# Kernel tuning notes

Measured on AMD Instinct MI355X. Metric: run time of the kernel, lower is better.

Reference implementation:

```python
import jax, jax.numpy as jnp
import numpy as np

N_GAUSS, H, W, SH_DEG = 1024, 256, 256, 3

SH_C0 = 0.28209479177387814
SH_C1 = 0.4886025119029199
SH_C2 = (1.0925484305920792, -1.0925484305920792, 0.31539156525252005,
         -1.0925484305920792, 0.5462742152960396)
SH_C3 = (-0.5900435899266435, 2.890611442640554, -0.4570457994644658,
         0.3731763325901154, -0.4570457994644658, 1.445305721320277,
         -0.5900435899266435)


def eval_sh(shs, dirs):
    # shs: [N,16,3], dirs: [N,3] normalized. Matches computeColorFromSH (deg 3).
    x, y, z = dirs[:, 0:1], dirs[:, 1:2], dirs[:, 2:3]
    res = SH_C0 * shs[:, 0]
    res = res - SH_C1 * y * shs[:, 1] + SH_C1 * z * shs[:, 2] - SH_C1 * x * shs[:, 3]
    xx, yy, zz = x * x, y * y, z * z
    xy, yz, xz = x * y, y * z, x * z
    res = (res + SH_C2[0] * xy * shs[:, 4] + SH_C2[1] * yz * shs[:, 5]
           + SH_C2[2] * (2.0 * zz - xx - yy) * shs[:, 6]
           + SH_C2[3] * xz * shs[:, 7] + SH_C2[4] * (xx - yy) * shs[:, 8])
    res = (res + SH_C3[0] * y * (3.0 * xx - yy) * shs[:, 9]
           + SH_C3[1] * xy * z * shs[:, 10]
           + SH_C3[2] * y * (4.0 * zz - xx - yy) * shs[:, 11]
           + SH_C3[3] * z * (2.0 * zz - 3.0 * xx - 3.0 * yy) * shs[:, 12]
           + SH_C3[4] * x * (4.0 * zz - xx - yy) * shs[:, 13]
           + SH_C3[5] * z * (xx - yy) * shs[:, 14]
           + SH_C3[6] * x * (xx - yy - zz) * shs[:, 15])
    return jnp.maximum(res + 0.5, 0.0)


def render(background, means3D, opacities, scales, rotations, shs,
           view_mat, proj_mat, cam_pos, tan_fovx, tan_fovy, height, width):
    N = means3D.shape[0]
    tanx, tany = tan_fovx[0], tan_fovy[0]
    fx = width / (2.0 * tanx)
    fy = height / (2.0 * tany)

    # --- 3D covariance: Sigma = R diag(s^2) R^T (computeCov3D) ---
    q = rotations / jnp.linalg.norm(rotations, axis=-1, keepdims=True)
    r, x, y, z = q[:, 0], q[:, 1], q[:, 2], q[:, 3]
    R = jnp.stack([
        jnp.stack([1 - 2 * (y * y + z * z), 2 * (x * y - r * z), 2 * (x * z + r * y)], -1),
        jnp.stack([2 * (x * y + r * z), 1 - 2 * (x * x + z * z), 2 * (y * z - r * x)], -1),
        jnp.stack([2 * (x * z - r * y), 2 * (y * z + r * x), 1 - 2 * (x * x + y * y)], -1),
    ], -2)  # [N,3,3]
    M = R * scales[:, None, :]
    Sigma = jnp.einsum('nij,nkj->nik', M, M)  # [N,3,3]

    # --- view transform + EWA 2D covariance (computeCov2D) ---
    t = means3D @ view_mat[:3, :3].T + view_mat[:3, 3]  # [N,3] camera space
    tz = t[:, 2]
    valid_z = tz > 0.2
    tzs = jnp.where(valid_z, tz, 1.0)
    limx, limy = 1.3 * tanx, 1.3 * tany
    tx = jnp.clip(t[:, 0] / tzs, -limx, limx) * tzs
    ty = jnp.clip(t[:, 1] / tzs, -limy, limy) * tzs
    zeros = jnp.zeros_like(tzs)
    J = jnp.stack([
        jnp.stack([fx / tzs, zeros, -fx * tx / (tzs * tzs)], -1),
        jnp.stack([zeros, fy / tzs, -fy * ty / (tzs * tzs)], -1),
    ], -2)  # [N,2,3]
    T2 = jnp.einsum('nij,jk->nik', J, view_mat[:3, :3])
    cov2d = jnp.einsum('nij,njk,nlk->nil', T2, Sigma, T2)  # [N,2,2]
    a = cov2d[:, 0, 0] + 0.3
    c = cov2d[:, 1, 1] + 0.3
    b = cov2d[:, 0, 1]
    det = a * c - b * b
    valid = valid_z & (det > 0)
    inv_det = jnp.where(det > 0, 1.0 / jnp.where(det > 0, det, 1.0), 0.0)
    conic = jnp.stack([c, -b, a], -1) * inv_det[:, None]  # [N,3]

    # --- projection to pixel coords (ndc2Pix) ---
    ph = jnp.concatenate([means3D, jnp.ones((N, 1), means3D.dtype)], -1) @ proj_mat.T
    p_w = 1.0 / (ph[:, 3] + 1e-7)
    px = ((ph[:, 0] * p_w + 1.0) * width - 1.0) * 0.5
    py = ((ph[:, 1] * p_w + 1.0) * height - 1.0) * 0.5

    # --- SH -> RGB ---
    dirs = means3D - cam_pos[None, :]
    dirs = dirs / jnp.linalg.norm(dirs, axis=-1, keepdims=True)
    colors = eval_sh(shs, dirs)  # [N,3]

    # --- global depth sort (front to back) ---
    depth = jnp.where(valid, tz, 1e10)
    order = jnp.argsort(depth)
    px_s, py_s = px[order], py[order]
    conic_s = conic[order]
    opac_s = opacities[order, 0]
    colors_s = colors[order]
    valid_s = valid[order]

    # --- per-pixel alpha and front-to-back compositing (renderCUDA) ---
    ys, xs = jnp.meshgrid(jnp.arange(height, dtype=jnp.float32),
                          jnp.arange(width, dtype=jnp.float32), indexing='ij')
    pixx, pixy = xs.reshape(-1), ys.reshape(-1)  # [P]
    dx = px_s[:, None] - pixx[None, :]  # [N,P]
    dy = py_s[:, None] - pixy[None, :]
    power = (-0.5 * (conic_s[:, 0:1] * dx * dx + conic_s[:, 2:3] * dy * dy)
             - conic_s[:, 1:2] * dx * dy)
    alpha = jnp.minimum(opac_s[:, None] * jnp.exp(jnp.minimum(power, 0.0)), 0.99)
    keep = (power <= 0.0) & (alpha >= 1.0 / 255.0) & valid_s[:, None]
    alpha = jnp.where(keep, alpha, 0.0)

    Tcum = jnp.cumprod(1.0 - alpha, axis=0)  # [N,P]
    T_prev = jnp.concatenate([jnp.ones((1, alpha.shape[1]), alpha.dtype), Tcum[:-1]], 0)
    wgt = alpha * T_prev
    img = jnp.einsum('nc,np->cp', colors_s, wgt) + background[:, None] * Tcum[-1][None, :]
    return img.reshape(3, height, width)


def setup_inputs() -> dict:
    key = jax.random.key(0)
    ks = jax.random.split(key, 6)
    means3D = jax.random.uniform(ks[0], (N_GAUSS, 3), minval=-3.0, maxval=3.0)
    means3D = means3D.at[:, 2].set(
        jax.random.uniform(ks[1], (N_GAUSS,), minval=2.0, maxval=10.0))
    opacities = jax.random.uniform(ks[2], (N_GAUSS, 1), minval=0.3, maxval=0.95)
    scales = jax.random.uniform(ks[3], (N_GAUSS, 3), minval=0.02, maxval=0.15)
    rotations = jax.random.normal(ks[4], (N_GAUSS, 4))
    shs = jax.random.normal(ks[5], (N_GAUSS, (SH_DEG + 1) ** 2, 3)) * 0.3
    background = jnp.zeros((3,), jnp.float32)
    view_mat = jnp.eye(4, dtype=jnp.float32)  # camera at origin looking +z
    tanx = tany = 0.5
    zn, zf = 0.01, 100.0
    proj = np.zeros((4, 4), np.float32)
    proj[0, 0] = 1.0 / tanx
    proj[1, 1] = 1.0 / tany
    proj[2, 2] = zf / (zf - zn)
    proj[2, 3] = -(zf * zn) / (zf - zn)
    proj[3, 2] = 1.0
    proj_mat = jnp.asarray(proj) @ view_mat  # full projection
    cam_pos = jnp.zeros((3,), jnp.float32)
    return dict(background=background, means3D=means3D, opacities=opacities,
                scales=scales, rotations=rotations, shs=shs, view_mat=view_mat,
                proj_mat=proj_mat, cam_pos=cam_pos,
                tan_fovx=jnp.array([tanx], jnp.float32),
                tan_fovy=jnp.array([tany], jnp.float32), height=H, width=W)


def reference(background, means3D, opacities, scales, rotations, shs,
              view_mat, proj_mat, cam_pos, tan_fovx, tan_fovy, height, width):
    return render(background, means3D, opacities, scales, rotations, shs,
                  view_mat, proj_mat, cam_pos, tan_fovx, tan_fovy, height, width)
```

## Files before the change

kernel.cpp:

```cpp
#include <hip/hip_runtime.h>
#include <math.h>

#define NG 1024
#define LOG2E 1.4426950408889634f


__global__ void prep_kernel(
    const float* __restrict__ means3D, const float* __restrict__ opacities,
    const float* __restrict__ scales,  const float* __restrict__ rotations,
    const float* __restrict__ shs,     const float* __restrict__ view_mat,
    const float* __restrict__ proj_mat,const float* __restrict__ cam_pos,
    const float* __restrict__ tanx_p,  const float* __restrict__ tany_p,
    const int* __restrict__ h_p,       const int* __restrict__ w_p,
    unsigned long long* __restrict__ keys, float4* __restrict__ bbox,
    float4* __restrict__ rec, int N)
{
    int i = blockIdx.x * blockDim.x + threadIdx.x;
    if (i >= N) return;
    float tanx = tanx_p[0], tany = tany_p[0];
    float Wf = (float)w_p[0], Hf = (float)h_p[0];
    float fx = Wf / (2.f * tanx), fy = Hf / (2.f * tany);

    float mx = means3D[3*i], my = means3D[3*i+1], mz = means3D[3*i+2];

    float qr = rotations[4*i],   qx = rotations[4*i+1];
    float qy = rotations[4*i+2], qz = rotations[4*i+3];
    float qn = sqrtf(qr*qr + qx*qx + qy*qy + qz*qz);
    qr /= qn; qx /= qn; qy /= qn; qz /= qn;
    float sx = scales[3*i], sy = scales[3*i+1], sz = scales[3*i+2];
    float R00 = 1.f-2.f*(qy*qy+qz*qz), R01 = 2.f*(qx*qy-qr*qz), R02 = 2.f*(qx*qz+qr*qy);
    float R10 = 2.f*(qx*qy+qr*qz), R11 = 1.f-2.f*(qx*qx+qz*qz), R12 = 2.f*(qy*qz-qr*qx);
    float R20 = 2.f*(qx*qz-qr*qy), R21 = 2.f*(qy*qz+qr*qx), R22 = 1.f-2.f*(qx*qx+qy*qy);
    float M00=R00*sx, M01=R01*sy, M02=R02*sz;
    float M10=R10*sx, M11=R11*sy, M12=R12*sz;
    float M20=R20*sx, M21=R21*sy, M22=R22*sz;
    float S00 = M00*M00+M01*M01+M02*M02;
    float S01 = M00*M10+M01*M11+M02*M12;
    float S02 = M00*M20+M01*M21+M02*M22;
    float S11 = M10*M10+M11*M11+M12*M12;
    float S12 = M10*M20+M11*M21+M12*M22;
    float S22 = M20*M20+M21*M21+M22*M22;

    const float* V = view_mat;
    float t0 = V[0]*mx + V[1]*my + V[2]*mz  + V[3];
    float t1 = V[4]*mx + V[5]*my + V[6]*mz  + V[7];
    float t2 = V[8]*mx + V[9]*my + V[10]*mz + V[11];
    bool valid_z = t2 > 0.2f;
    float tzs = valid_z ? t2 : 1.0f;
    float limx = 1.3f*tanx, limy = 1.3f*tany;
    float txc = fminf(fmaxf(t0/tzs, -limx), limx) * tzs;
    float tyc = fminf(fmaxf(t1/tzs, -limy), limy) * tzs;
    float inv_tz = 1.f / tzs;
    float J00 = fx*inv_tz, J02 = -fx*txc*inv_tz*inv_tz;
    float J11 = fy*inv_tz, J12 = -fy*tyc*inv_tz*inv_tz;
    float T200 = J00*V[0] + J02*V[8];
    float T201 = J00*V[1] + J02*V[9];
    float T202 = J00*V[2] + J02*V[10];
    float T210 = J11*V[4] + J12*V[8];
    float T211 = J11*V[5] + J12*V[9];
    float T212 = J11*V[6] + J12*V[10];
    float u0 = S00*T200 + S01*T201 + S02*T202;
    float u1 = S01*T200 + S11*T201 + S12*T202;
    float u2 = S02*T200 + S12*T201 + S22*T202;
    float cov00 = T200*u0 + T201*u1 + T202*u2;
    float cov01 = T210*u0 + T211*u1 + T212*u2;
    float v0 = S00*T210 + S01*T211 + S02*T212;
    float v1 = S01*T210 + S11*T211 + S12*T212;
    float v2 = S02*T210 + S12*T211 + S22*T212;
    float cov11 = T210*v0 + T211*v1 + T212*v2;
    float a = cov00 + 0.3f;
    float c = cov11 + 0.3f;
    float b = cov01;
    float det = a*c - b*b;
    bool valid = valid_z && (det > 0.f);
    float inv_det = (det > 0.f) ? (1.f/det) : 0.f;
    float Aq = c*inv_det, Bq = -b*inv_det, Cq = a*inv_det;

    const float* P = proj_mat;
    float ph0 = P[0]*mx  + P[1]*my  + P[2]*mz  + P[3];
    float ph1 = P[4]*mx  + P[5]*my  + P[6]*mz  + P[7];
    float ph3 = P[12]*mx + P[13]*my + P[14]*mz + P[15];
    float pw = 1.f / (ph3 + 1e-7f);
    float px = ((ph0*pw + 1.f)*Wf - 1.f)*0.5f;
    float py = ((ph1*pw + 1.f)*Hf - 1.f)*0.5f;

    float dxm = mx - cam_pos[0], dym = my - cam_pos[1], dzm = mz - cam_pos[2];
    float dn = sqrtf(dxm*dxm + dym*dym + dzm*dzm);
    float X = dxm/dn, Y = dym/dn, Z = dzm/dn;
    float xx = X*X, yy = Y*Y, zz = Z*Z;
    float xy = X*Y, yz = Y*Z, xz = X*Z;
    float col[3];
    #pragma unroll
    for (int ch = 0; ch < 3; ch++) {
        const float* s = shs + i*48 + ch;
        float res = 0.28209479177387814f * s[0];
        res += -0.4886025119029199f * Y * s[3]
             +  0.4886025119029199f * Z * s[6]
             -  0.4886025119029199f * X * s[9];
        res +=  1.0925484305920792f * xy * s[12]
             + (-1.0925484305920792f) * yz * s[15]
             +  0.31539156525252005f * (2.f*zz - xx - yy) * s[18]
             + (-1.0925484305920792f) * xz * s[21]
             +  0.5462742152960396f * (xx - yy) * s[24];
        res += -0.5900435899266435f * Y * (3.f*xx - yy) * s[27]
             +  2.890611442640554f  * xy * Z * s[30]
             + (-0.4570457994644658f) * Y * (4.f*zz - xx - yy) * s[33]
             +  0.3731763325901154f  * Z * (2.f*zz - 3.f*xx - 3.f*yy) * s[36]
             + (-0.4570457994644658f) * X * (4.f*zz - xx - yy) * s[39]
             +  1.445305721320277f   * Z * (xx - yy) * s[42]
             + (-0.5900435899266435f) * X * (xx - yy - zz) * s[45];
        col[ch] = fmaxf(res + 0.5f, 0.f);
    }

    float op = valid ? opacities[i] : 0.f;
    float dpt = valid ? t2 : 1e10f;
    keys[i] = ((unsigned long long)__float_as_uint(dpt) << 32) | (unsigned)i;

    float tau = 2.f * logf(255.f * fmaxf(op, 1e-20f));
    bool has = valid && (op * 255.f > 1.f) && (tau > 0.f);
    float rx = has ? (sqrtf(tau * a) + 0.01f) : 0.f;
    float ry = has ? (sqrtf(tau * c) + 0.01f) : 0.f;
    bbox[i] = has ? make_float4(px - rx, py - ry, px + rx, py + ry)
                  : make_float4(1e9f, 1e9f, -1e9f, -1e9f);

    rec[i*3 + 0] = make_float4(px, py, -0.5f*LOG2E*Aq, -LOG2E*Bq);
    rec[i*3 + 1] = make_float4(-0.5f*LOG2E*Cq, op, col[0], col[1]);
    rec[i*3 + 2] = make_float4(col[2], 0.f, 0.f, 0.f);
}

__device__ inline unsigned long long bstage_shfl(unsigned long long key,
                                                 int tid, int j, int k) {
    unsigned long long partner = __shfl_xor(key, j, 64);
    bool lower = (tid & j) == 0;
    bool asc   = (tid & k) == 0;
    return ((key < partner) == (lower == asc)) ? key : partner;
}

__device__ inline float rlane(float v, int l) {
    return __int_as_float(__builtin_amdgcn_readlane(__float_as_int(v), l));
}

__global__ void __launch_bounds__(64) render_kernel(
    const unsigned long long* __restrict__ keys,
    const float4* __restrict__ bbox,
    const float4* __restrict__ rec,
    const float* __restrict__ background,
    float* __restrict__ out,
    int N, int W, int HW)
{
    __shared__ unsigned long long skey[NG];
    int tile = blockIdx.x;
    int tilesX = W >> 3;
    int tx = tile % tilesX, ty = tile / tilesX;
    int lane = threadIdx.x;
    int lx = lane & 7, ly = lane >> 3;
    float pixx = (float)(tx*8 + lx);
    float pixy = (float)(ty*8 + ly);
    float x0 = (float)(tx*8), x1 = x0 + 7.f;
    float y0 = (float)(ty*8), y1 = y0 + 7.f;

    int cnt = 0;
    for (int base = 0; base < N; base += 64) {
        int gi = base + lane;
        bool hit = false;
        unsigned long long k = 0;
        if (gi < N) {
            float4 bb = bbox[gi];
            k = keys[gi];
            hit = (bb.x <= x1) & (bb.z >= x0) & (bb.y <= y1) & (bb.w >= y0);
        }
        unsigned long long mask = __ballot(hit);
        if (hit) {
            int pos = cnt + __popcll(mask & ((1ull << lane) - 1ull));
            skey[pos] = k;
        }
        cnt += __popcll(mask);
    }
    __syncthreads();

    float T = 1.f, Cr = 0.f, Cg = 0.f, Cb = 0.f;
    if (cnt > 0) {
        if (cnt <= 64) {
            unsigned long long key = (lane < cnt) ? skey[lane] : ~0ull;
            for (int k = 2; k <= 64; k <<= 1)
                for (int j = k >> 1; j >= 1; j >>= 1)
                    key = bstage_shfl(key, lane, j, k);
            skey[lane] = key;
            __syncthreads();
        } else {
            int P = 128;
            while (P < cnt) P <<= 1;
            for (int i2 = cnt + lane; i2 < P; i2 += 64) skey[i2] = ~0ull;
            __syncthreads();
            for (int k = 2; k <= P; k <<= 1) {
                for (int j = k >> 1; j >= 1; j >>= 1) {
                    for (int i2 = lane; i2 < P; i2 += 64) {
                        int ixj = i2 ^ j;
                        if (ixj > i2) {
                            bool asc = (i2 & k) == 0;
                            unsigned long long u = skey[i2], v = skey[ixj];
                            if ((u > v) == asc) { skey[i2] = v; skey[ixj] = u; }
                        }
                    }
                    __syncthreads();
                }
            }
        }

        bool dead = false;
        for (int c = 0; c < cnt && !dead; c += 64) {
            int len = min(64, cnt - c);
            int idx = c + lane;
            int gg = (idx < cnt) ? (int)(unsigned)skey[idx] : 0;
            float4 r0 = rec[gg*3 + 0];
            float4 r1 = rec[gg*3 + 1];
            float4 r2 = rec[gg*3 + 2];
            for (int m = 0; m < len; m++) {
                float gpx = rlane(r0.x, m), gpy = rlane(r0.y, m);
                float gA  = rlane(r0.z, m), gB  = rlane(r0.w, m);
                float gC  = rlane(r1.x, m), gop = rlane(r1.y, m);
                float gcr = rlane(r1.z, m), gcg = rlane(r1.w, m);
                float gcb = rlane(r2.x, m);
                float dx = gpx - pixx, dy = gpy - pixy;
                float p2 = fmaf(gA, dx*dx, fmaf(gC, dy*dy, gB*(dx*dy)));
                float e  = __builtin_amdgcn_exp2f(p2);
                float alpha = fminf(gop * e, 0.99f);
                float a2 = (alpha >= (1.f/255.f)) ? alpha : 0.f;
                float w = a2 * T;
                Cr = fmaf(gcr, w, Cr);
                Cg = fmaf(gcg, w, Cg);
                Cb = fmaf(gcb, w, Cb);
                T  = T - a2 * T;
                if ((m & 15) == 15 && __all(T < 1e-4f)) { dead = true; break; }
            }
            if (__all(T < 1e-4f)) dead = true;
        }
    }

    int p = (ty*8 + ly) * W + tx*8 + lx;
    out[p]        = Cr + background[0]*T;
    out[HW + p]   = Cg + background[1]*T;
    out[2*HW + p] = Cb + background[2]*T;
}

extern "C" void kernel_launch(void* const* d_in, const int* in_sizes, int n_in,
                              void* d_out, int out_size, void* d_ws, size_t ws_size,
                              hipStream_t stream) {
    const float* background = (const float*)d_in[0];
    const float* means3D    = (const float*)d_in[1];
    const float* opacities  = (const float*)d_in[2];
    const float* scales     = (const float*)d_in[3];
    const float* rotations  = (const float*)d_in[4];
    const float* shs        = (const float*)d_in[5];
    const float* view_mat   = (const float*)d_in[6];
    const float* proj_mat   = (const float*)d_in[7];
    const float* cam_pos    = (const float*)d_in[8];
    const float* tanx       = (const float*)d_in[9];
    const float* tany       = (const float*)d_in[10];
    const int*   hp         = (const int*)d_in[11];
    const int*   wp         = (const int*)d_in[12];

    int N  = in_sizes[2];
    int HW = out_size / 3;
    int W  = 256;
    int H  = HW / W;
    float* out = (float*)d_out;

    unsigned long long* keys = (unsigned long long*)d_ws;
    float4* bbox = (float4*)(keys + NG);
    float4* rec  = bbox + NG;

    prep_kernel<<<16, 64, 0, stream>>>(
        means3D, opacities, scales, rotations, shs, view_mat, proj_mat,
        cam_pos, tanx, tany, hp, wp, keys, bbox, rec, N);

    int tiles = (W >> 3) * (H >> 3);
    render_kernel<<<tiles, 64, 0, stream>>>(
        keys, bbox, rec, background, out, N, W, HW);
}
```

Baseline: 20.56 us.

## Precompute per-Gaussian tile ranges and pack keys into one record

The prep kernel now computes each Gaussian's integer tile range, packed into 8-bit fields, and writes it with the depth key into a single uint4 record. This replaces the separate 64-bit key and float4 bbox arrays. The render kernel loads four records per lane per iteration and culls with integer compares instead of float bbox tests. A dedicated fast path handles tiles with at most 64 hits, keeping the sorted key in a register and blending without a shared-memory round trip, and SH coefficients and rotations are read with vectorized float4 loads. The 8-bit packing assumes at most 255 tiles per axis.

```diff
diff --git a/kernel.cpp b/kernel.cpp
--- a/kernel.cpp
+++ b/kernel.cpp
@@ -12,19 +12,19 @@
     const float* __restrict__ proj_mat,const float* __restrict__ cam_pos,
     const float* __restrict__ tanx_p,  const float* __restrict__ tany_p,
     const int* __restrict__ h_p,       const int* __restrict__ w_p,
-    unsigned long long* __restrict__ keys, float4* __restrict__ bbox,
-    float4* __restrict__ rec, int N)
+    uint4* __restrict__ grec, float4* __restrict__ rec, int N)
 {
     int i = blockIdx.x * blockDim.x + threadIdx.x;
     if (i >= N) return;
     float tanx = tanx_p[0], tany = tany_p[0];
     float Wf = (float)w_p[0], Hf = (float)h_p[0];
+    int tilesX = w_p[0] >> 3, tilesY = h_p[0] >> 3;
     float fx = Wf / (2.f * tanx), fy = Hf / (2.f * tany);
 
     float mx = means3D[3*i], my = means3D[3*i+1], mz = means3D[3*i+2];
 
-    float qr = rotations[4*i],   qx = rotations[4*i+1];
-    float qy = rotations[4*i+2], qz = rotations[4*i+3];
+    float4 q4 = ((const float4*)rotations)[i];
+    float qr = q4.x, qx = q4.y, qy = q4.z, qz = q4.w;
     float qn = sqrtf(qr*qr + qx*qx + qy*qy + qz*qz);
     qr /= qn; qx /= qn; qy /= qn; qz /= qn;
     float sx = scales[3*i], sy = scales[3*i+1], sz = scales[3*i+2];
@@ -89,39 +89,58 @@
     float X = dxm/dn, Y = dym/dn, Z = dzm/dn;
     float xx = X*X, yy = Y*Y, zz = Z*Z;
     float xy = X*Y, yz = Y*Z, xz = X*Z;
+    float sc[48];
+    {
+        const float4* s4 = (const float4*)(shs + i*48);
+        #pragma unroll
+        for (int k = 0; k < 12; k++) {
+            float4 v = s4[k];
+            sc[4*k] = v.x; sc[4*k+1] = v.y; sc[4*k+2] = v.z; sc[4*k+3] = v.w;
+        }
+    }
     float col[3];
     #pragma unroll
     for (int ch = 0; ch < 3; ch++) {
-        const float* s = shs + i*48 + ch;
-        float res = 0.28209479177387814f * s[0];
-        res += -0.4886025119029199f * Y * s[3]
-             +  0.4886025119029199f * Z * s[6]
-             -  0.4886025119029199f * X * s[9];
-        res +=  1.0925484305920792f * xy * s[12]
-             + (-1.0925484305920792f) * yz * s[15]
-             +  0.31539156525252005f * (2.f*zz - xx - yy) * s[18]
-             + (-1.0925484305920792f) * xz * s[21]
-             +  0.5462742152960396f * (xx - yy) * s[24];
-        res += -0.5900435899266435f * Y * (3.f*xx - yy) * s[27]
-             +  2.890611442640554f  * xy * Z * s[30]
-             + (-0.4570457994644658f) * Y * (4.f*zz - xx - yy) * s[33]
-             +  0.3731763325901154f  * Z * (2.f*zz - 3.f*xx - 3.f*yy) * s[36]
-             + (-0.4570457994644658f) * X * (4.f*zz - xx - yy) * s[39]
-             +  1.445305721320277f   * Z * (xx - yy) * s[42]
-             + (-0.5900435899266435f) * X * (xx - yy - zz) * s[45];
+        float res = 0.28209479177387814f * sc[ch];
+        res += -0.4886025119029199f * Y * sc[3+ch]
+             +  0.4886025119029199f * Z * sc[6+ch]
+             -  0.4886025119029199f * X * sc[9+ch];
+        res +=  1.0925484305920792f * xy * sc[12+ch]
+             + (-1.0925484305920792f) * yz * sc[15+ch]
+             +  0.31539156525252005f * (2.f*zz - xx - yy) * sc[18+ch]
+             + (-1.0925484305920792f) * xz * sc[21+ch]
+             +  0.5462742152960396f * (xx - yy) * sc[24+ch];
+        res += -0.5900435899266435f * Y * (3.f*xx - yy) * sc[27+ch]
+             +  2.890611442640554f  * xy * Z * sc[30+ch]
+             + (-0.4570457994644658f) * Y * (4.f*zz - xx - yy) * sc[33+ch]
+             +  0.3731763325901154f  * Z * (2.f*zz - 3.f*xx - 3.f*yy) * sc[36+ch]
+             + (-0.4570457994644658f) * X * (4.f*zz - xx - yy) * sc[39+ch]
+             +  1.445305721320277f   * Z * (xx - yy) * sc[42+ch]
+             + (-0.5900435899266435f) * X * (xx - yy - zz) * sc[45+ch];
         col[ch] = fmaxf(res + 0.5f, 0.f);
     }
 
     float op = valid ? opacities[i] : 0.f;
     float dpt = valid ? t2 : 1e10f;
-    keys[i] = ((unsigned long long)__float_as_uint(dpt) << 32) | (unsigned)i;
 
     float tau = 2.f * logf(255.f * fmaxf(op, 1e-20f));
     bool has = valid && (op * 255.f > 1.f) && (tau > 0.f);
     float rx = has ? (sqrtf(tau * a) + 0.01f) : 0.f;
     float ry = has ? (sqrtf(tau * c) + 0.01f) : 0.f;
-    bbox[i] = has ? make_float4(px - rx, py - ry, px + rx, py + ry)
-                  : make_float4(1e9f, 1e9f, -1e9f, -1e9f);
+
+    unsigned trange = 255u;
+    if (has) {
+        int tx0 = (int)ceilf((px - rx - 7.f) * 0.125f);
+        int tx1 = (int)floorf((px + rx) * 0.125f);
+        int ty0 = (int)ceilf((py - ry - 7.f) * 0.125f);
+        int ty1 = (int)floorf((py + ry) * 0.125f);
+        tx0 = max(tx0, 0); ty0 = max(ty0, 0);
+        tx1 = min(tx1, tilesX - 1); ty1 = min(ty1, tilesY - 1);
+        if (tx0 <= tx1 && ty0 <= ty1)
+            trange = (unsigned)tx0 | ((unsigned)tx1 << 8)
+                   | ((unsigned)ty0 << 16) | ((unsigned)ty1 << 24);
+    }
+    grec[i] = make_uint4(__float_as_uint(dpt), (unsigned)i, trange, 0u);
 
     rec[i*3 + 0] = make_float4(px, py, -0.5f*LOG2E*Aq, -LOG2E*Bq);
     rec[i*3 + 1] = make_float4(-0.5f*LOG2E*Cq, op, col[0], col[1]);
@@ -141,8 +160,7 @@
 }
 
 __global__ void __launch_bounds__(64) render_kernel(
-    const unsigned long long* __restrict__ keys,
-    const float4* __restrict__ bbox,
+    const uint4* __restrict__ grec,
     const float4* __restrict__ rec,
     const float* __restrict__ background,
     float* __restrict__ out,
@@ -156,57 +174,77 @@
     int lx = lane & 7, ly = lane >> 3;
     float pixx = (float)(tx*8 + lx);
     float pixy = (float)(ty*8 + ly);
-    float x0 = (float)(tx*8), x1 = x0 + 7.f;
-    float y0 = (float)(ty*8), y1 = y0 + 7.f;
 
     int cnt = 0;
-    for (int base = 0; base < N; base += 64) {
-        int gi = base + lane;
-        bool hit = false;
-        unsigned long long k = 0;
-        if (gi < N) {
-            float4 bb = bbox[gi];
-            k = keys[gi];
-            hit = (bb.x <= x1) & (bb.z >= x0) & (bb.y <= y1) & (bb.w >= y0);
-        }
-        unsigned long long mask = __ballot(hit);
-        if (hit) {
-            int pos = cnt + __popcll(mask & ((1ull << lane) - 1ull));
-            skey[pos] = k;
-        }
-        cnt += __popcll(mask);
+    const uint4 miss = make_uint4(0u, 0u, 255u, 0u);
+    for (int base = 0; base < N; base += 256) {
+        int g0 = base + lane;
+        uint4 ra = (g0       < N) ? grec[g0]       : miss;
+        uint4 rb = (g0 + 64  < N) ? grec[g0 + 64]  : miss;
+        uint4 rc = (g0 + 128 < N) ? grec[g0 + 128] : miss;
+        uint4 rd = (g0 + 192 < N) ? grec[g0 + 192] : miss;
+        #pragma unroll
+        for (int s = 0; s < 4; s++) {
+            uint4 r = (s == 0) ? ra : (s == 1) ? rb : (s == 2) ? rc : rd;
+            unsigned tr = r.z;
+            bool hit = (tx >= (int)(tr & 255u)) & (tx <= (int)((tr >> 8) & 255u))
+                     & (ty >= (int)((tr >> 16) & 255u)) & (ty <= (int)(tr >> 24));
+            unsigned long long mask = __ballot(hit);
+            if (hit) {
+                int pos = cnt + __popcll(mask & ((1ull << lane) - 1ull));
+                skey[pos] = ((unsigned long long)r.x << 32) | r.y;
+            }
+            cnt += __popcll(mask);
+        }
     }
     __syncthreads();
 
     float T = 1.f, Cr = 0.f, Cg = 0.f, Cb = 0.f;
-    if (cnt > 0) {
-        if (cnt <= 64) {
-            unsigned long long key = (lane < cnt) ? skey[lane] : ~0ull;
-            for (int k = 2; k <= 64; k <<= 1)
-                for (int j = k >> 1; j >= 1; j >>= 1)
-                    key = bstage_shfl(key, lane, j, k);
-            skey[lane] = key;
-            __syncthreads();
-        } else {
-            int P = 128;
-            while (P < cnt) P <<= 1;
-            for (int i2 = cnt + lane; i2 < P; i2 += 64) skey[i2] = ~0ull;
-            __syncthreads();
-            for (int k = 2; k <= P; k <<= 1) {
-                for (int j = k >> 1; j >= 1; j >>= 1) {
-                    for (int i2 = lane; i2 < P; i2 += 64) {
-                        int ixj = i2 ^ j;
-                        if (ixj > i2) {
-                            bool asc = (i2 & k) == 0;
-                            unsigned long long u = skey[i2], v = skey[ixj];
-                            if ((u > v) == asc) { skey[i2] = v; skey[ixj] = u; }
-                        }
+    if (cnt > 0 && cnt <= 64) {
+        unsigned long long key = (lane < cnt) ? skey[lane] : ~0ull;
+        for (int k = 2; k <= 64; k <<= 1)
+            for (int j = k >> 1; j >= 1; j >>= 1)
+                key = bstage_shfl(key, lane, j, k);
+        int gg = (lane < cnt) ? (int)(unsigned)key : 0;
+        float4 r0 = rec[gg*3 + 0];
+        float4 r1 = rec[gg*3 + 1];
+        float4 r2 = rec[gg*3 + 2];
+        for (int m = 0; m < cnt; m++) {
+            float gpx = rlane(r0.x, m), gpy = rlane(r0.y, m);
+            float gA  = rlane(r0.z, m), gB  = rlane(r0.w, m);
+            float gC  = rlane(r1.x, m), gop = rlane(r1.y, m);
+            float gcr = rlane(r1.z, m), gcg = rlane(r1.w, m);
+            float gcb = rlane(r2.x, m);
+            float dx = gpx - pixx, dy = gpy - pixy;
+            float p2 = fmaf(gA, dx*dx, fmaf(gC, dy*dy, gB*(dx*dy)));
+            float e  = __builtin_amdgcn_exp2f(p2);
+            float alpha = fminf(gop * e, 0.99f);
+            float a2 = (alpha >= (1.f/255.f)) ? alpha : 0.f;
+            float w = a2 * T;
+            Cr = fmaf(gcr, w, Cr);
+            Cg = fmaf(gcg, w, Cg);
+            Cb = fmaf(gcb, w, Cb);
+            T  = T - a2 * T;
+            if ((m & 15) == 15 && __all(T < 1e-4f)) break;
+        }
+    } else if (cnt > 64) {
+        int P = 128;
+        while (P < cnt) P <<= 1;
+        for (int i2 = cnt + lane; i2 < P; i2 += 64) skey[i2] = ~0ull;
+        __syncthreads();
+        for (int k = 2; k <= P; k <<= 1) {
+            for (int j = k >> 1; j >= 1; j >>= 1) {
+                for (int i2 = lane; i2 < P; i2 += 64) {
+                    int ixj = i2 ^ j;
+                    if (ixj > i2) {
+                        bool asc = (i2 & k) == 0;
+                        unsigned long long u = skey[i2], v = skey[ixj];
+                        if ((u > v) == asc) { skey[i2] = v; skey[ixj] = u; }
                     }
-                    __syncthreads();
                 }
+                __syncthreads();
             }
         }
-
         bool dead = false;
         for (int c = 0; c < cnt && !dead; c += 64) {
             int len = min(64, cnt - c);
@@ -266,15 +304,14 @@
     int H  = HW / W;
     float* out = (float*)d_out;
 
-    unsigned long long* keys = (unsigned long long*)d_ws;
-    float4* bbox = (float4*)(keys + NG);
-    float4* rec  = bbox + NG;
+    uint4*  grec = (uint4*)d_ws;
+    float4* rec  = (float4*)(grec + NG);
 
     prep_kernel<<<16, 64, 0, stream>>>(
         means3D, opacities, scales, rotations, shs, view_mat, proj_mat,
-        cam_pos, tanx, tany, hp, wp, keys, bbox, rec, N);
+        cam_pos, tanx, tany, hp, wp, grec, rec, N);
 
     int tiles = (W >> 3) * (H >> 3);
     render_kernel<<<tiles, 64, 0, stream>>>(
-        keys, bbox, rec, background, out, N, W, HW);
-}
+        grec, rec, background, out, N, W, HW);
+}
```

Measured after the change: 21.78 us. +5.9%, slower.
